# Kernel tuning notes

Measured on AMD Instinct MI355X. Metric: run time of the kernel, lower is better.

## Reference

```python
import jax, jax.numpy as jnp
import numpy as np

B, C, H, W = 4, 256, 96, 96
PARA, MOD, NH = 256, 256, 128
PI = 3.14159  # constant used in the torch source (not math.pi)


def setup_inputs():
    key = jax.random.key(0)
    ks = jax.random.split(key, 16)
    w = lambda k, shp: jax.random.normal(k, shp, jnp.float32) * 0.02
    z = lambda n: jnp.zeros((n,), jnp.float32)
    return {
        "feature_map": jax.random.normal(ks[0], (B, C, H, W), jnp.float32),
        "para_code": jax.random.normal(ks[1], (B, PARA), jnp.float32),
        "style_code": jax.random.normal(ks[2], (B, MOD), jnp.float32),
        "lin_common_w": w(ks[3], (PARA, PARA)), "lin_common_b": z(PARA),
        "lin_scale_w": w(ks[4], (PARA, C)), "lin_scale_b": z(C),
        "lin_rot_w": w(ks[5], (PARA, C)), "lin_rot_b": z(C),
        "lin_trans_w": w(ks[6], (PARA, 2 * C)), "lin_trans_b": z(2 * C),
        "a1_shared_w": w(ks[7], (MOD, NH)), "a1_shared_b": z(NH),
        "a1_gamma_w": w(ks[8], (NH, C)), "a1_gamma_b": z(C),
        "a1_beta_w": w(ks[9], (NH, C)), "a1_beta_b": z(C),
        "conv1_w": w(ks[10], (C, C, 3, 3)), "conv1_b": z(C),
        "a2_shared_w": w(ks[11], (MOD, NH)), "a2_shared_b": z(NH),
        "a2_gamma_w": w(ks[12], (NH, C)), "a2_gamma_b": z(C),
        "a2_beta_w": w(ks[13], (NH, C)), "a2_beta_b": z(C),
        "conv2_w": w(ks[14], (C, C, 3, 3)), "conv2_b": z(C),
    }


def _adaat(fm, pc, cw, cb, sw, sb, rw, rb, tw, tb):
    # fm: [B,C,H,W]; per-channel 2D affine warp, channels act as depth of a 3D grid_sample.
    Bn, Cn, Hn, Wn = fm.shape
    pc = jax.nn.relu(pc @ cw + cb)
    scale = jax.nn.sigmoid(pc @ sw + sb) * 2.0            # [B,C]
    angle = jnp.tanh(pc @ rw + rb) * PI                   # [B,C]
    trans = jnp.tanh(pc @ tw + tb).reshape(Bn, Cn, 2)     # [B,C,2]
    cos = jnp.cos(angle)[:, :, None, None]
    sin = jnp.sin(angle)[:, :, None, None]
    sc = scale[:, :, None, None]
    tx = trans[:, :, 0][:, :, None, None]
    ty = trans[:, :, 1][:, :, None, None]
    # align_corners=True style normalized source grid (as in make_coordinate_grid_3d)
    gx = (2.0 * jnp.arange(Wn) / (Wn - 1) - 1.0)[None, :]  # [1,W]
    gy = (2.0 * jnp.arange(Hn) / (Hn - 1) - 1.0)[:, None]  # [H,1]
    # rotation [[cos,-sin],[sin,cos]] @ [x,y], then scale + translate -> [B,C,H,W]
    xw = (cos * gx - sin * gy) * sc + tx
    yw = (sin * gx + cos * gy) * sc + ty
    gz = 2.0 * jnp.arange(Cn) / (Cn - 1) - 1.0             # [C]
    # unnormalize with align_corners=False (torch grid_sample default)
    ix = ((xw + 1.0) * Wn - 1.0) * 0.5
    iy = ((yw + 1.0) * Hn - 1.0) * 0.5
    iz = (((gz + 1.0) * Cn - 1.0) * 0.5)[None, :, None, None]  # [1,C,1,1]
    x0 = jnp.floor(ix); y0 = jnp.floor(iy); z0 = jnp.floor(iz)
    wx = ix - x0; wy = iy - y0; wz = iz - z0
    x0 = x0.astype(jnp.int32); y0 = y0.astype(jnp.int32); z0 = z0.astype(jnp.int32)
    bidx = jnp.arange(Bn)[:, None, None, None]

    def gather(zi, yi, xi):
        valid = (zi >= 0) & (zi < Cn) & (yi >= 0) & (yi < Hn) & (xi >= 0) & (xi < Wn)
        v = fm[bidx, jnp.clip(zi, 0, Cn - 1), jnp.clip(yi, 0, Hn - 1), jnp.clip(xi, 0, Wn - 1)]
        return jnp.where(valid, v, 0.0)

    out = jnp.zeros_like(fm)
    for dz, wzc in ((0, 1.0 - wz), (1, wz)):
        for dy, wyc in ((0, 1.0 - wy), (1, wy)):
            for dx, wxc in ((0, 1.0 - wx), (1, wx)):
                out = out + gather(z0 + dz, y0 + dy, x0 + dx) * (wzc * wyc * wxc)
    return out


def _adain_layer(x, style, shw, shb, gw, gb, bw, bb):
    m = x.mean(axis=(2, 3), keepdims=True)
    v = x.var(axis=(2, 3), keepdims=True)  # biased, as torch InstanceNorm2d
    xn = (x - m) / jnp.sqrt(v + 1e-5)
    a = jax.nn.relu(style @ shw + shb)
    gamma = (a @ gw + gb)[:, :, None, None]
    beta = (a @ bw + bb)[:, :, None, None]
    return xn * (1.0 + gamma) + beta


def _conv3(x, w, b):
    y = jax.lax.conv_general_dilated(x, w, (1, 1), ((1, 1), (1, 1)),
                                     dimension_numbers=("NCHW", "OIHW", "NCHW"))
    return y + b[None, :, None, None]


def _lrelu(x):
    return jnp.where(x >= 0, x, 0.2 * x)


def reference(feature_map, para_code, style_code,
              lin_common_w, lin_common_b, lin_scale_w, lin_scale_b,
              lin_rot_w, lin_rot_b, lin_trans_w, lin_trans_b,
              a1_shared_w, a1_shared_b, a1_gamma_w, a1_gamma_b, a1_beta_w, a1_beta_b,
              conv1_w, conv1_b,
              a2_shared_w, a2_shared_b, a2_gamma_w, a2_gamma_b, a2_beta_w, a2_beta_b,
              conv2_w, conv2_b):
    t = _adaat(feature_map, para_code, lin_common_w, lin_common_b,
               lin_scale_w, lin_scale_b, lin_rot_w, lin_rot_b, lin_trans_w, lin_trans_b)
    x = _adain_layer(t, style_code, a1_shared_w, a1_shared_b, a1_gamma_w, a1_gamma_b, a1_beta_w, a1_beta_b)
    x = _conv3(_lrelu(x), conv1_w, conv1_b)
    x = _adain_layer(x, style_code, a2_shared_w, a2_shared_b, a2_gamma_w, a2_gamma_b, a2_beta_w, a2_beta_b)
    x = _conv3(_lrelu(x), conv2_w, conv2_b)
    return x
```

## Files before the change

### kernel.cpp

```cpp
#include <hip/hip_runtime.h>
#include <hip/hip_bf16.h>
#include <cstddef>

#define BATCH 4
#define CH 256
#define HH 96
#define WW 96
#define HWN (HH*WW)
#define NTOT (BATCH*CH*HWN)
#define XT_H 98
#define XT_W 98
#define XT_PLANE (XT_H*XT_W*CH)

typedef __attribute__((ext_vector_type(16))) float f32x16;
typedef __attribute__((ext_vector_type(8))) __bf16 bfrag;
typedef __attribute__((ext_vector_type(8))) unsigned short u16x8;

static __device__ __forceinline__ unsigned short f2bf(float f) {
  unsigned int u = __float_as_uint(f);
  unsigned int r = (u + 0x7fffu + ((u >> 16) & 1u)) >> 16;
  return (unsigned short)r;
}
static __device__ __forceinline__ float bf2f(unsigned short s) {
  return __uint_as_float(((unsigned int)s) << 16);
}

static __device__ __forceinline__ void gload16(const unsigned short* g,
                                               unsigned short* l) {
  __builtin_amdgcn_global_load_lds(
      (const __attribute__((address_space(1))) unsigned int*)g,
      (__attribute__((address_space(3))) unsigned int*)l, 16, 0, 0);
}

__global__ __launch_bounds__(256) void params_stage1_kernel(
    const float* __restrict__ para, const float* __restrict__ style,
    const float* __restrict__ cw,  const float* __restrict__ cb,
    const float* __restrict__ a1w, const float* __restrict__ a1b,
    const float* __restrict__ a2w, const float* __restrict__ a2b,
    float* __restrict__ pcbuf, float* __restrict__ a1buf, float* __restrict__ a2buf)
{
  __shared__ float s_in[256];
  __shared__ float red[256];
  int part = blockIdx.x, b = blockIdx.y, t = threadIdx.x;
  s_in[t] = (part < 4) ? para[b*256 + t] : style[b*256 + t];
  __syncthreads();
  if (part < 4) {
    int o = t & 63, ks = t >> 6, co0 = part * 64;
    const float* wcol = cw + co0 + o;
    float acc = 0.f;
    #pragma unroll 8
    for (int i = 0; i < 64; i++) {
      int k = ks * 64 + i;
      acc = fmaf(s_in[k], wcol[k * 256], acc);
    }
    red[t] = acc;
    __syncthreads();
    if (t < 64) {
      float s = red[t] + red[t + 64] + red[t + 128] + red[t + 192];
      pcbuf[b*256 + co0 + t] = fmaxf(s + cb[co0 + t], 0.f);
    }
  } else {
    const float* w  = (part == 4) ? a1w : a2w;
    const float* bb = (part == 4) ? a1b : a2b;
    float* outp = (part == 4) ? a1buf : a2buf;
    int o = t & 127, ks = t >> 7;
    const float* wcol = w + o;
    float acc = 0.f;
    #pragma unroll 8
    for (int i = 0; i < 128; i++) {
      int k = ks * 128 + i;
      acc = fmaf(s_in[k], wcol[k * 128], acc);
    }
    red[t] = acc;
    __syncthreads();
    if (t < 128) {
      float s = red[t] + red[t + 128];
      outp[b*128 + t] = fmaxf(s + bb[t], 0.f);
    }
  }
}

__global__ __launch_bounds__(256) void params_stage2_kernel(
    const float* __restrict__ pcbuf, const float* __restrict__ a1buf,
    const float* __restrict__ a2buf,
    const float* __restrict__ sw,  const float* __restrict__ sb,
    const float* __restrict__ rw,  const float* __restrict__ rb,
    const float* __restrict__ tw,  const float* __restrict__ tb,
    const float* __restrict__ g1w, const float* __restrict__ g1b,
    const float* __restrict__ b1w, const float* __restrict__ b1b,
    const float* __restrict__ g2w, const float* __restrict__ g2b,
    const float* __restrict__ b2w, const float* __restrict__ b2b,
    float* __restrict__ warp, float* __restrict__ gb1, float* __restrict__ gb2)
{
  __shared__ float s_pc[256], s_a1[128], s_a2[128];
  __shared__ float red[8][4][16];
  int co0 = blockIdx.x * 16, b = blockIdx.y, t = threadIdx.x;
  s_pc[t] = pcbuf[b*256 + t];
  if (t < 128) s_a1[t] = a1buf[b*128 + t];
  else         s_a2[t - 128] = a2buf[b*128 + (t - 128)];
  __syncthreads();

  int cl = t & 15, klane = t >> 4;
  int c = co0 + cl;
  const float2* tw2 = (const float2*)tw;
  float ds = 0.f, dr = 0.f, dtx = 0.f, dty = 0.f;
  float g1 = 0.f, be1 = 0.f, g2 = 0.f, be2 = 0.f;
  #pragma unroll 4
  for (int kk = 0; kk < 16; kk++) {
    int i = klane * 16 + kk;
    float p = s_pc[i];
    ds  = fmaf(p, sw[i*256 + c], ds);
    dr  = fmaf(p, rw[i*256 + c], dr);
    float2 tv = tw2[i*256 + c];
    dtx = fmaf(p, tv.x, dtx);
    dty = fmaf(p, tv.y, dty);
  }
  #pragma unroll 4
  for (int kk = 0; kk < 8; kk++) {
    int i = klane * 8 + kk;
    float a = s_a1[i];
    g1  = fmaf(a, g1w[i*256 + c], g1);
    be1 = fmaf(a, b1w[i*256 + c], be1);
    float a2v = s_a2[i];
    g2  = fmaf(a2v, g2w[i*256 + c], g2);
    be2 = fmaf(a2v, b2w[i*256 + c], be2);
  }
  ds  += __shfl_down(ds, 32, 64);  ds  += __shfl_down(ds, 16, 64);
  dr  += __shfl_down(dr, 32, 64);  dr  += __shfl_down(dr, 16, 64);
  dtx += __shfl_down(dtx, 32, 64); dtx += __shfl_down(dtx, 16, 64);
  dty += __shfl_down(dty, 32, 64); dty += __shfl_down(dty, 16, 64);
  g1  += __shfl_down(g1, 32, 64);  g1  += __shfl_down(g1, 16, 64);
  be1 += __shfl_down(be1, 32, 64); be1 += __shfl_down(be1, 16, 64);
  g2  += __shfl_down(g2, 32, 64);  g2  += __shfl_down(g2, 16, 64);
  be2 += __shfl_down(be2, 32, 64); be2 += __shfl_down(be2, 16, 64);
  int wv = t >> 6;
  if ((t & 63) < 16) {
    red[0][wv][cl] = ds;  red[1][wv][cl] = dr;
    red[2][wv][cl] = dtx; red[3][wv][cl] = dty;
    red[4][wv][cl] = g1;  red[5][wv][cl] = be1;
    red[6][wv][cl] = g2;  red[7][wv][cl] = be2;
  }
  __syncthreads();
  if (t < 16) {
    float v[8];
    #pragma unroll
    for (int o = 0; o < 8; o++)
      v[o] = red[o][0][t] + red[o][1][t] + red[o][2][t] + red[o][3][t];
    int cc = co0 + t;
    int bc = b*256 + cc;
    float scale = 2.f / (1.f + expf(-(v[0] + sb[cc])));
    float ang = tanhf(v[1] + rb[cc]) * 3.14159f;
    float sn, cs;
    sincosf(ang, &sn, &cs);
    warp[bc*4 + 0] = cs * scale;
    warp[bc*4 + 1] = sn * scale;
    warp[bc*4 + 2] = tanhf(v[2] + tb[2*cc]);
    warp[bc*4 + 3] = tanhf(v[3] + tb[2*cc + 1]);
    gb1[bc*2]     = v[4] + g1b[cc];
    gb1[bc*2 + 1] = v[5] + b1b[cc];
    gb2[bc*2]     = v[6] + g2b[cc];
    gb2[bc*2 + 1] = v[7] + b2b[cc];
  }
}

__global__ __launch_bounds__(256) void prep_weights_kernel(
    const float* __restrict__ w1, const float* __restrict__ w2,
    unsigned short* __restrict__ wf1, unsigned short* __restrict__ wf2)
{
  int co = blockIdx.x & 255;
  const float* src = (blockIdx.x < 256) ? w1 : w2;
  unsigned short* dst = (blockIdx.x < 256) ? wf1 : wf2;
  int ci = threadIdx.x;
  int coblk = co >> 6, m = (co >> 5) & 1;
  int l = (co & 31) | (((ci >> 3) & 1) << 5);
  int ks = ci >> 4, j = ci & 7;
  const float* p = src + ((size_t)co * 256 + ci) * 9;
  #pragma unroll
  for (int tap = 0; tap < 9; tap++) {
    size_t idx = (((size_t)((coblk * 16 + ks) * 9 + tap) * 2 + m) * 64 + l) * 8 + j;
    dst[idx] = f2bf(p[tap]);
  }
}

__global__ __launch_bounds__(256) void adaat_kernel(
    const float* __restrict__ fm, const float* __restrict__ warp,
    const float* __restrict__ gb1, float* __restrict__ tout,
    float* __restrict__ nrm1)
{
  __shared__ float s[96 * 100];
  int bc = blockIdx.x;
  int b = bc >> 8, c = bc & 255;
  float csc = warp[bc*4 + 0], ssc = warp[bc*4 + 1];
  float tx = warp[bc*4 + 2], ty = warp[bc*4 + 3];

  const float axw = csc * (96.f / 95.f);
  const float axh = -ssc * (96.f / 95.f);
  const float ax0 = 48.f * (tx - csc + ssc) + 47.5f;
  const float ayw = ssc * (96.f / 95.f);
  const float ayh = csc * (96.f / 95.f);
  const float ay0 = 48.f * (ty - ssc - csc) + 47.5f;

  float iz = 256.f * (float)c / 255.f - 0.5f;
  float z0f = floorf(iz);
  float wz = iz - z0f;
  int z0 = (int)z0f;
  const float* p0 = (z0 >= 0) ? fm + (size_t)(b*256 + z0) * HWN : nullptr;
  const float* p1 = (z0 + 1 < 256) ? fm + (size_t)(b*256 + z0 + 1) * HWN : nullptr;
  float w0 = 1.f - wz, w1 = wz;

  int t = threadIdx.x;
  const float4* q0 = (const float4*)p0;
  const float4* q1 = (const float4*)p1;
  for (int i = t; i < 2304; i += 256) {
    int row = i / 24, col = i - row * 24;
    float4 r = {0.f, 0.f, 0.f, 0.f};
    if (q0) {
      float4 v = q0[i];
      r.x = w0 * v.x; r.y = w0 * v.y; r.z = w0 * v.z; r.w = w0 * v.w;
    }
    if (q1) {
      float4 v = q1[i];
      r.x = fmaf(w1, v.x, r.x); r.y = fmaf(w1, v.y, r.y);
      r.z = fmaf(w1, v.z, r.z); r.w = fmaf(w1, v.w, r.w);
    }
    *(float4*)&s[row * 100 + col * 4] = r;
  }
  __syncthreads();

  int h = t / 96, w = t - (t / 96) * 96;
  float* dst = tout + (size_t)bc * HWN;
  float sum = 0.f, sumsq = 0.f;
  #pragma unroll
  for (int k = 0; k < 36; k++) {
    float ix = fmaf(axw, (float)w, fmaf(axh, (float)h, ax0));
    float iy = fmaf(ayw, (float)w, fmaf(ayh, (float)h, ay0));
    float x0f = floorf(ix), y0f = floorf(iy);
    float wx = ix - x0f, wy = iy - y0f;
    int x0 = (int)x0f, y0 = (int)y0f;
    int x0c = min(max(x0, 0), 95), x1c = min(max(x0 + 1, 0), 95);
    int y0c = min(max(y0, 0), 95), y1c = min(max(y0 + 1, 0), 95);
    bool vx0 = (unsigned)x0 < 96u, vx1 = (unsigned)(x0 + 1) < 96u;
    bool vy0 = (unsigned)y0 < 96u, vy1 = (unsigned)(y0 + 1) < 96u;
    float a00 = s[y0c * 100 + x0c], a01 = s[y0c * 100 + x1c];
    float a10 = s[y1c * 100 + x0c], a11 = s[y1c * 100 + x1c];
    float wxm = 1.f - wx, wym = 1.f - wy;
    float w00 = (vy0 && vx0) ? wym * wxm : 0.f;
    float w01 = (vy0 && vx1) ? wym * wx  : 0.f;
    float w10 = (vy1 && vx0) ? wy * wxm  : 0.f;
    float w11 = (vy1 && vx1) ? wy * wx   : 0.f;
    float v = w00 * a00;
    v = fmaf(w01, a01, v);
    v = fmaf(w10, a10, v);
    v = fmaf(w11, a11, v);
    dst[t + k * 256] = v;
    sum += v;
    sumsq = fmaf(v, v, sumsq);
    int wn = w + 64;
    int carry = (wn >= 96) ? 1 : 0;
    w = wn - (carry ? 96 : 0);
    h += 2 + carry;
  }

  for (int off = 32; off > 0; off >>= 1) {
    sum   += __shfl_down(sum, off, 64);
    sumsq += __shfl_down(sumsq, off, 64);
  }
  __shared__ float rs[4], rq[4];
  int lane = t & 63, wvi = t >> 6;
  if (lane == 0) { rs[wvi] = sum; rq[wvi] = sumsq; }
  __syncthreads();
  if (t == 0) {
    float S = rs[0] + rs[1] + rs[2] + rs[3];
    float Q = rq[0] + rq[1] + rq[2] + rq[3];
    float m = S * (1.f / 9216.f);
    float var = Q * (1.f / 9216.f) - m * m;
    float rstd = rsqrtf(var + 1e-5f);
    float sc = (1.f + gb1[bc*2]) * rstd;
    nrm1[bc*2] = sc;
    nrm1[bc*2 + 1] = gb1[bc*2 + 1] - m * sc;
  }
}

__global__ __launch_bounds__(256) void finalize_stats_kernel(
    const float* __restrict__ psum, const float* __restrict__ gb,
    float* __restrict__ nrm)
{
  int bc = blockIdx.x * 256 + threadIdx.x;
  int b = bc >> 8, co = bc & 255;
  float S = 0.f, Q = 0.f;
  for (int j = 0; j < 96; j++) {
    const float* p = psum + ((((size_t)b * 48 + (j >> 1)) * 2 + (j & 1)) * 256 + co) * 2;
    S += p[0];
    Q += p[1];
  }
  float m = S * (1.f / 9216.f);
  float var = Q * (1.f / 9216.f) - m * m;
  float rstd = rsqrtf(var + 1e-5f);
  float sc = (1.f + gb[bc*2]) * rstd;
  nrm[bc*2] = sc;
  nrm[bc*2 + 1] = gb[bc*2 + 1] - m * sc;
}

__global__ __launch_bounds__(256) void transpose_norm_kernel(
    const float* __restrict__ x, const float* __restrict__ nrm,
    unsigned short* __restrict__ xt)
{
  int hi = blockIdx.x;
  int b  = blockIdx.y;
  unsigned short* dst = xt + (size_t)b * XT_PLANE + (size_t)hi * (XT_W * CH);
  int t = threadIdx.x;
  int h = hi - 1;
  u16x8 zero = {0,0,0,0,0,0,0,0};
  if (h < 0 || h >= 96) {
    for (int c = t; c < XT_W * CH / 8; c += 256) ((u16x8*)dst)[c] = zero;
    return;
  }
  __shared__ unsigned short s[96 * 256];
  int ci = t;
  float sc = nrm[(b*256 + ci)*2], bi = nrm[(b*256 + ci)*2 + 1];
  const float* src = x + ((size_t)(b*256 + ci)) * HWN + h * 96;
  for (int wg = 0; wg < 24; wg++) {
    float4 v = *(const float4*)(src + wg * 4);
    float y0 = fmaf(v.x, sc, bi); y0 = (y0 >= 0.f) ? y0 : 0.2f * y0;
    float y1 = fmaf(v.y, sc, bi); y1 = (y1 >= 0.f) ? y1 : 0.2f * y1;
    float y2 = fmaf(v.z, sc, bi); y2 = (y2 >= 0.f) ? y2 : 0.2f * y2;
    float y3 = fmaf(v.w, sc, bi); y3 = (y3 >= 0.f) ? y3 : 0.2f * y3;
    s[(wg*4 + 0) * 256 + ci] = f2bf(y0);
    s[(wg*4 + 1) * 256 + ci] = f2bf(y1);
    s[(wg*4 + 2) * 256 + ci] = f2bf(y2);
    s[(wg*4 + 3) * 256 + ci] = f2bf(y3);
  }
  __syncthreads();
  for (int c = t; c < 98 * 32; c += 256) {
    int w = c >> 5, p = c & 31;
    u16x8 v = zero;
    if (w >= 1 && w <= 96) v = *(const u16x8*)&s[(w - 1) * 256 + p * 8];
    ((u16x8*)dst)[c] = v;
  }
}

__global__ __launch_bounds__(256) void norm2_kernel(
    unsigned short* __restrict__ xt, const float* __restrict__ nrm)
{
  int hi = blockIdx.x, b = blockIdx.y;
  unsigned short* row = xt + (size_t)b * XT_PLANE + (size_t)hi * (XT_W * CH);
  int t = threadIdx.x;
  u16x8 zero = {0,0,0,0,0,0,0,0};
  if (hi == 0 || hi == 97) {
    for (int c = t; c < XT_W * CH / 8; c += 256) ((u16x8*)row)[c] = zero;
    return;
  }
  int p = t & 31;
  float sc[8], bi[8];
  #pragma unroll
  for (int j = 0; j < 8; j++) {
    int co = p * 8 + j;
    sc[j] = nrm[(b*256 + co)*2];
    bi[j] = nrm[(b*256 + co)*2 + 1];
  }
  for (int wi = t >> 5; wi < 98; wi += 8) {
    int c = wi * 32 + p;
    if (wi == 0 || wi == 97) { ((u16x8*)row)[c] = zero; continue; }
    u16x8 v = ((u16x8*)row)[c];
    u16x8 o;
    #pragma unroll
    for (int j = 0; j < 8; j++) {
      float x = bf2f(v[j]);
      float y = fmaf(x, sc[j], bi[j]);
      y = (y >= 0.f) ? y : 0.2f * y;
      o[j] = f2bf(y);
    }
    ((u16x8*)row)[c] = o;
  }
}

__global__ __launch_bounds__(256, 3) void conv_mfma_kernel(
    const unsigned short* __restrict__ xt,
    const unsigned short* __restrict__ wf,
    const float* __restrict__ cb,
    float* __restrict__ out,
    unsigned short* __restrict__ xt2,
    float* __restrict__ psum)
{
  __shared__ __align__(16) unsigned short s_in[2][6528];

  int hb = blockIdx.x, coblk = blockIdx.y, b = blockIdx.z;
  int co0 = coblk * 64, h0 = hb * 2;
  int t = threadIdx.x, lane = t & 63, wv = t >> 6;
  int rw = wv >> 1, mh = wv & 1;
  int l31 = lane & 31, lhi = lane >> 5;
  const unsigned short* xtb = xt + (size_t)b * XT_PLANE;

  int pre_g[4];
  #pragma unroll
  for (int i = 0; i < 4; i++) {
    int c = t + i * 256;
    if (c < 784) {
      int r = c / 196;
      int rem = c - r * 196;
      int half = rem / 98;
      int w = rem - half * 98;
      pre_g[i] = ((h0 + r) * 98 + w) * 256 + half * 8;
    }
  }

  f32x16 acc[3];
  #pragma unroll
  for (int n = 0; n < 3; n++)
    #pragma unroll
    for (int i = 0; i < 16; i++) acc[n][i] = 0.f;

  const unsigned short* wfb = wf + (size_t)(coblk * 16) * 9216 + mh * 512 + lane * 8;

  {
    #pragma unroll
    for (int i = 0; i < 3; i++)
      gload16(xtb + pre_g[i], &s_in[0][(i * 256 + wv * 64) * 8]);
    u16x8 tail0;
    if (t < 16) tail0 = *(const u16x8*)(xtb + pre_g[3]);
    if (t < 16) *(u16x8*)(&s_in[0][(768 + t) * 8]) = tail0;
  }
  bfrag wa[9];
  #pragma unroll
  for (int tap = 0; tap < 9; tap++) wa[tap] = *(const bfrag*)(wfb + tap * 1024);
  __syncthreads();

  int buf = 0;
  u16x8 tail;
  #pragma unroll 1
  for (int ks = 0; ks < 16; ks++) {
    if (ks < 15) {
      int cib = (ks + 1) * 16;
      unsigned short* nb = s_in[buf ^ 1];
      #pragma unroll
      for (int i = 0; i < 3; i++)
        gload16(xtb + pre_g[i] + cib, &nb[(i * 256 + wv * 64) * 8]);
      if (t < 16) tail = *(const u16x8*)(xtb + pre_g[3] + cib);
    }
    const unsigned short* sb = s_in[buf];
    int ksn = (ks < 15) ? (ks + 1) : 15;
    const unsigned short* wkn = wfb + (size_t)ksn * 9216;
    #pragma unroll
    for (int ky = 0; ky < 3; ky++) {
      const unsigned short* srow = sb + (((rw + ky) * 2 + lhi) * 98) * 8;
      bfrag bb[9];
      #pragma unroll
      for (int kx = 0; kx < 3; kx++)
        #pragma unroll
        for (int n = 0; n < 3; n++)
          bb[kx * 3 + n] = *(const bfrag*)(srow + (n * 32 + kx + l31) * 8);
      __builtin_amdgcn_s_setprio(1);
      #pragma unroll
      for (int kx = 0; kx < 3; kx++) {
        int tap = ky * 3 + kx;
        acc[0] = __builtin_amdgcn_mfma_f32_32x32x16_bf16(wa[tap], bb[kx*3+0], acc[0], 0, 0, 0);
        acc[1] = __builtin_amdgcn_mfma_f32_32x32x16_bf16(wa[tap], bb[kx*3+1], acc[1], 0, 0, 0);
        acc[2] = __builtin_amdgcn_mfma_f32_32x32x16_bf16(wa[tap], bb[kx*3+2], acc[2], 0, 0, 0);
        wa[tap] = *(const bfrag*)(wkn + tap * 1024);
      }
      __builtin_amdgcn_s_setprio(0);
    }
    if (ks < 15 && t < 16) *(u16x8*)(&s_in[buf ^ 1][(768 + t) * 8]) = tail;
    __syncthreads();
    buf ^= 1;
  }

  int h = h0 + rw;
  if (psum) {
    unsigned short* tb = (unsigned short*)s_in;
    float bsum[16], bsq[16];
    #pragma unroll
    for (int r = 0; r < 16; r++) {
      int row = (r & 3) + 8 * (r >> 2) + 4 * lhi;
      int col = mh * 32 + row;
      float bv = cb[co0 + col];
      float s = 0.f, q = 0.f;
      #pragma unroll
      for (int n = 0; n < 3; n++) {
        float y = acc[n][r] + bv;
        int px = n * 32 + l31;
        tb[(rw * 96 + px) * 68 + col] = f2bf(y);
        s += y;
        q = fmaf(y, y, q);
      }
      bsum[r] = s; bsq[r] = q;
    }
    #pragma unroll
    for (int r = 0; r < 16; r++) {
      float s = bsum[r], q = bsq[r];
      #pragma unroll
      for (int off = 16; off > 0; off >>= 1) {
        s += __shfl_xor(s, off, 64);
        q += __shfl_xor(q, off, 64);
      }
      bsum[r] = s; bsq[r] = q;
    }
    if (l31 == 0) {
      float* pp = psum + ((((size_t)b * 48 + hb) * 2 + rw) * 256) * 2;
      #pragma unroll
      for (int r = 0; r < 16; r++) {
        int row = (r & 3) + 8 * (r >> 2) + 4 * lhi;
        int co = co0 + mh * 32 + row;
        pp[co * 2]     = bsum[r];
        pp[co * 2 + 1] = bsq[r];
      }
    }
    __syncthreads();
    unsigned short* dstb = xt2 + (size_t)b * XT_PLANE;
    #pragma unroll
    for (int i = 0; i < 6; i++) {
      int c = t + i * 256;
      int row2 = c / 768;
      int rem = c - row2 * 768;
      int wi = rem >> 3, p8 = rem & 7;
      const unsigned short* lsrc = &tb[(row2 * 96 + wi) * 68 + p8 * 8];
      uint2 lo = *(const uint2*)lsrc;
      uint2 hi2 = *(const uint2*)(lsrc + 4);
      size_t ga = ((size_t)(h0 + 1 + row2) * 98 + (wi + 1)) * 256 + co0 + p8 * 8;
      uint4 vv; vv.x = lo.x; vv.y = lo.y; vv.z = hi2.x; vv.w = hi2.y;
      *(uint4*)&dstb[ga] = vv;
    }
  } else {
    #pragma unroll
    for (int r = 0; r < 16; r++) {
      int row = (r & 3) + 8 * (r >> 2) + 4 * lhi;
      int co = co0 + mh * 32 + row;
      float bv = cb[co];
      size_t base = ((size_t)(b * 256 + co) * 96 + h) * 96;
      #pragma unroll
      for (int n = 0; n < 3; n++) {
        out[base + n * 32 + l31] = acc[n][r] + bv;
      }
    }
  }
}

extern "C" void kernel_launch(void* const* d_in, const int* in_sizes, int n_in,
                              void* d_out, int out_size, void* d_ws, size_t ws_size,
                              hipStream_t stream)
{
  const float* fm    = (const float*)d_in[0];
  const float* para  = (const float*)d_in[1];
  const float* style = (const float*)d_in[2];
  const float* cw  = (const float*)d_in[3];
  const float* cb  = (const float*)d_in[4];
  const float* sw  = (const float*)d_in[5];
  const float* sb  = (const float*)d_in[6];
  const float* rw  = (const float*)d_in[7];
  const float* rb  = (const float*)d_in[8];
  const float* tw  = (const float*)d_in[9];
  const float* tb  = (const float*)d_in[10];
  const float* a1w = (const float*)d_in[11];
  const float* a1b = (const float*)d_in[12];
  const float* g1w = (const float*)d_in[13];
  const float* g1b = (const float*)d_in[14];
  const float* b1w = (const float*)d_in[15];
  const float* b1b = (const float*)d_in[16];
  const float* c1w = (const float*)d_in[17];
  const float* c1b = (const float*)d_in[18];
  const float* a2w = (const float*)d_in[19];
  const float* a2b = (const float*)d_in[20];
  const float* g2w = (const float*)d_in[21];
  const float* g2b = (const float*)d_in[22];
  const float* b2w = (const float*)d_in[23];
  const float* b2b = (const float*)d_in[24];
  const float* c2w = (const float*)d_in[25];
  const float* c2b = (const float*)d_in[26];

  float* outf = (float*)d_out;

  unsigned short* xtbuf  = (unsigned short*)d_ws;
  unsigned short* xt2buf = xtbuf + (size_t)BATCH * XT_PLANE;
  unsigned short* wf1    = xt2buf + (size_t)BATCH * XT_PLANE;
  unsigned short* wf2    = wf1 + 9 * 256 * 256;
  float* fws  = (float*)(wf2 + 9 * 256 * 256);
  float* warp = fws;
  float* gb1  = warp + 4 * 1024;
  float* gb2  = gb1 + 2 * 1024;
  float* nrm1 = gb2 + 2 * 1024;
  float* nrm2 = nrm1 + 2 * 1024;
  float* pcbuf = nrm2 + 2 * 1024;
  float* a1buf = pcbuf + 1024;
  float* a2buf = a1buf + 512;
  float* psum  = a2buf + 512;

  params_stage1_kernel<<<dim3(6, 4), 256, 0, stream>>>(para, style, cw, cb,
      a1w, a1b, a2w, a2b, pcbuf, a1buf, a2buf);
  params_stage2_kernel<<<dim3(16, 4), 256, 0, stream>>>(pcbuf, a1buf, a2buf,
      sw, sb, rw, rb, tw, tb, g1w, g1b, b1w, b1b, g2w, g2b, b2w, b2b,
      warp, gb1, gb2);
  prep_weights_kernel<<<512, 256, 0, stream>>>(c1w, c2w, wf1, wf2);
  adaat_kernel<<<1024, 256, 0, stream>>>(fm, warp, gb1, outf, nrm1);
  transpose_norm_kernel<<<dim3(98, 4), 256, 0, stream>>>(outf, nrm1, xtbuf);
  conv_mfma_kernel<<<dim3(48, 4, 4), 256, 0, stream>>>(xtbuf, wf1, c1b,
      outf, xt2buf, psum);
  finalize_stats_kernel<<<4, 256, 0, stream>>>(psum, gb2, nrm2);
  norm2_kernel<<<dim3(98, 4), 256, 0, stream>>>(xt2buf, nrm2);
  conv_mfma_kernel<<<dim3(48, 4, 4), 256, 0, stream>>>(xt2buf, wf2, c2b,
      outf, nullptr, nullptr);
}
```

Baseline: 185.1 us.

## Fuse AdaIN-1 normalize into adaat kernel, store bf16, remap conv block order

The adaat kernel now keeps its 36 warped values per thread in registers. After the block reduction it applies the AdaIN scale/bias and leaky ReLU itself, then writes bf16 instead of fp32. The transpose kernel becomes a pure bf16 transpose, which halves the intermediate traffic, and the nrm1 buffer is removed. The conv kernels switch to a 1D grid with a custom index decode that interleaves co-blocks and batch pairs, aiming at better L2 reuse of input rows and weights. The cost is higher register pressure in the adaat kernel and bf16 rounding earlier in the pipeline.

```diff
diff --git a/kernel.cpp b/kernel.cpp
--- a/kernel.cpp
+++ b/kernel.cpp
@@ -184,8 +184,7 @@
 
 __global__ __launch_bounds__(256) void adaat_kernel(
     const float* __restrict__ fm, const float* __restrict__ warp,
-    const float* __restrict__ gb1, float* __restrict__ tout,
-    float* __restrict__ nrm1)
+    const float* __restrict__ gb1, unsigned short* __restrict__ tout)
 {
   __shared__ float s[96 * 100];
   int bc = blockIdx.x;
@@ -228,7 +227,7 @@
   __syncthreads();
 
   int h = t / 96, w = t - (t / 96) * 96;
-  float* dst = tout + (size_t)bc * HWN;
+  float vals[36];
   float sum = 0.f, sumsq = 0.f;
   #pragma unroll
   for (int k = 0; k < 36; k++) {
@@ -252,7 +251,7 @@
     v = fmaf(w01, a01, v);
     v = fmaf(w10, a10, v);
     v = fmaf(w11, a11, v);
-    dst[t + k * 256] = v;
+    vals[k] = v;
     sum += v;
     sumsq = fmaf(v, v, sumsq);
     int wn = w + 64;
@@ -265,7 +264,7 @@
     sum   += __shfl_down(sum, off, 64);
     sumsq += __shfl_down(sumsq, off, 64);
   }
-  __shared__ float rs[4], rq[4];
+  __shared__ float rs[4], rq[4], sbi[2];
   int lane = t & 63, wvi = t >> 6;
   if (lane == 0) { rs[wvi] = sum; rq[wvi] = sumsq; }
   __syncthreads();
@@ -276,8 +275,17 @@
     float var = Q * (1.f / 9216.f) - m * m;
     float rstd = rsqrtf(var + 1e-5f);
     float sc = (1.f + gb1[bc*2]) * rstd;
-    nrm1[bc*2] = sc;
-    nrm1[bc*2 + 1] = gb1[bc*2 + 1] - m * sc;
+    sbi[0] = sc;
+    sbi[1] = gb1[bc*2 + 1] - m * sc;
+  }
+  __syncthreads();
+  float sc = sbi[0], bi = sbi[1];
+  unsigned short* dst = tout + (size_t)bc * HWN + t;
+  #pragma unroll
+  for (int k = 0; k < 36; k++) {
+    float y = fmaf(vals[k], sc, bi);
+    y = (y >= 0.f) ? y : 0.2f * y;
+    dst[k * 256] = f2bf(y);
   }
 }
 
@@ -301,9 +309,8 @@
   nrm[bc*2 + 1] = gb[bc*2 + 1] - m * sc;
 }
 
-__global__ __launch_bounds__(256) void transpose_norm_kernel(
-    const float* __restrict__ x, const float* __restrict__ nrm,
-    unsigned short* __restrict__ xt)
+__global__ __launch_bounds__(256) void transpose_kernel(
+    const unsigned short* __restrict__ tb, unsigned short* __restrict__ xt)
 {
   int hi = blockIdx.x;
   int b  = blockIdx.y;
@@ -317,18 +324,12 @@
   }
   __shared__ unsigned short s[96 * 256];
   int ci = t;
-  float sc = nrm[(b*256 + ci)*2], bi = nrm[(b*256 + ci)*2 + 1];
-  const float* src = x + ((size_t)(b*256 + ci)) * HWN + h * 96;
-  for (int wg = 0; wg < 24; wg++) {
-    float4 v = *(const float4*)(src + wg * 4);
-    float y0 = fmaf(v.x, sc, bi); y0 = (y0 >= 0.f) ? y0 : 0.2f * y0;
-    float y1 = fmaf(v.y, sc, bi); y1 = (y1 >= 0.f) ? y1 : 0.2f * y1;
-    float y2 = fmaf(v.z, sc, bi); y2 = (y2 >= 0.f) ? y2 : 0.2f * y2;
-    float y3 = fmaf(v.w, sc, bi); y3 = (y3 >= 0.f) ? y3 : 0.2f * y3;
-    s[(wg*4 + 0) * 256 + ci] = f2bf(y0);
-    s[(wg*4 + 1) * 256 + ci] = f2bf(y1);
-    s[(wg*4 + 2) * 256 + ci] = f2bf(y2);
-    s[(wg*4 + 3) * 256 + ci] = f2bf(y3);
+  const unsigned short* src = tb + ((size_t)(b*256 + ci)) * HWN + h * 96;
+  #pragma unroll
+  for (int wg = 0; wg < 12; wg++) {
+    u16x8 v = *(const u16x8*)(src + wg * 8);
+    #pragma unroll
+    for (int j = 0; j < 8; j++) s[(wg*8 + j) * 256 + ci] = v[j];
   }
   __syncthreads();
   for (int c = t; c < 98 * 32; c += 256) {
@@ -384,7 +385,13 @@
 {
   __shared__ __align__(16) unsigned short s_in[2][6528];
 
-  int hb = blockIdx.x, coblk = blockIdx.y, b = blockIdx.z;
+  int n = blockIdx.x;
+  int coblk = n & 3;
+  int bit2 = (n >> 2) & 1;
+  int j = n >> 3;
+  int hb = j % 48;
+  int b = (j / 48) * 2 + bit2;
+
   int co0 = coblk * 64, h0 = hb * 2;
   int t = threadIdx.x, lane = t & 63, wv = t >> 6;
   int rw = wv >> 1, mh = wv & 1;
@@ -406,9 +413,9 @@
 
   f32x16 acc[3];
   #pragma unroll
-  for (int n = 0; n < 3; n++)
-    #pragma unroll
-    for (int i = 0; i < 16; i++) acc[n][i] = 0.f;
+  for (int nn = 0; nn < 3; nn++)
+    #pragma unroll
+    for (int i = 0; i < 16; i++) acc[nn][i] = 0.f;
 
   const unsigned short* wfb = wf + (size_t)(coblk * 16) * 9216 + mh * 512 + lane * 8;
 
@@ -447,8 +454,8 @@
       #pragma unroll
       for (int kx = 0; kx < 3; kx++)
         #pragma unroll
-        for (int n = 0; n < 3; n++)
-          bb[kx * 3 + n] = *(const bfrag*)(srow + (n * 32 + kx + l31) * 8);
+        for (int nn = 0; nn < 3; nn++)
+          bb[kx * 3 + nn] = *(const bfrag*)(srow + (nn * 32 + kx + l31) * 8);
       __builtin_amdgcn_s_setprio(1);
       #pragma unroll
       for (int kx = 0; kx < 3; kx++) {
@@ -467,7 +474,7 @@
 
   int h = h0 + rw;
   if (psum) {
-    unsigned short* tb = (unsigned short*)s_in;
+    unsigned short* tbl = (unsigned short*)s_in;
     float bsum[16], bsq[16];
     #pragma unroll
     for (int r = 0; r < 16; r++) {
@@ -476,10 +483,10 @@
       float bv = cb[co0 + col];
       float s = 0.f, q = 0.f;
       #pragma unroll
-      for (int n = 0; n < 3; n++) {
-        float y = acc[n][r] + bv;
-        int px = n * 32 + l31;
-        tb[(rw * 96 + px) * 68 + col] = f2bf(y);
+      for (int nn = 0; nn < 3; nn++) {
+        float y = acc[nn][r] + bv;
+        int px = nn * 32 + l31;
+        tbl[(rw * 96 + px) * 68 + col] = f2bf(y);
         s += y;
         q = fmaf(y, y, q);
       }
@@ -513,7 +520,7 @@
       int row2 = c / 768;
       int rem = c - row2 * 768;
       int wi = rem >> 3, p8 = rem & 7;
-      const unsigned short* lsrc = &tb[(row2 * 96 + wi) * 68 + p8 * 8];
+      const unsigned short* lsrc = &tbl[(row2 * 96 + wi) * 68 + p8 * 8];
       uint2 lo = *(const uint2*)lsrc;
       uint2 hi2 = *(const uint2*)(lsrc + 4);
       size_t ga = ((size_t)(h0 + 1 + row2) * 98 + (wi + 1)) * 256 + co0 + p8 * 8;
@@ -528,8 +535,8 @@
       float bv = cb[co];
       size_t base = ((size_t)(b * 256 + co) * 96 + h) * 96;
       #pragma unroll
-      for (int n = 0; n < 3; n++) {
-        out[base + n * 32 + l31] = acc[n][r] + bv;
+      for (int nn = 0; nn < 3; nn++) {
+        out[base + nn * 32 + l31] = acc[nn][r] + bv;
       }
     }
   }
@@ -568,6 +575,7 @@
   const float* c2b = (const float*)d_in[26];
 
   float* outf = (float*)d_out;
+  unsigned short* tbf16 = (unsigned short*)d_out;
 
   unsigned short* xtbuf  = (unsigned short*)d_ws;
   unsigned short* xt2buf = xtbuf + (size_t)BATCH * XT_PLANE;
@@ -577,8 +585,7 @@
   float* warp = fws;
   float* gb1  = warp + 4 * 1024;
   float* gb2  = gb1 + 2 * 1024;
-  float* nrm1 = gb2 + 2 * 1024;
-  float* nrm2 = nrm1 + 2 * 1024;
+  float* nrm2 = gb2 + 2 * 1024;
   float* pcbuf = nrm2 + 2 * 1024;
   float* a1buf = pcbuf + 1024;
   float* a2buf = a1buf + 512;
@@ -590,12 +597,12 @@
       sw, sb, rw, rb, tw, tb, g1w, g1b, b1w, b1b, g2w, g2b, b2w, b2b,
       warp, gb1, gb2);
   prep_weights_kernel<<<512, 256, 0, stream>>>(c1w, c2w, wf1, wf2);
-  adaat_kernel<<<1024, 256, 0, stream>>>(fm, warp, gb1, outf, nrm1);
-  transpose_norm_kernel<<<dim3(98, 4), 256, 0, stream>>>(outf, nrm1, xtbuf);
-  conv_mfma_kernel<<<dim3(48, 4, 4), 256, 0, stream>>>(xtbuf, wf1, c1b,
+  adaat_kernel<<<1024, 256, 0, stream>>>(fm, warp, gb1, tbf16);
+  transpose_kernel<<<dim3(98, 4), 256, 0, stream>>>(tbf16, xtbuf);
+  conv_mfma_kernel<<<768, 256, 0, stream>>>(xtbuf, wf1, c1b,
       outf, xt2buf, psum);
   finalize_stats_kernel<<<4, 256, 0, stream>>>(psum, gb2, nrm2);
   norm2_kernel<<<dim3(98, 4), 256, 0, stream>>>(xt2buf, nrm2);
-  conv_mfma_kernel<<<dim3(48, 4, 4), 256, 0, stream>>>(xt2buf, wf2, c2b,
+  conv_mfma_kernel<<<768, 256, 0, stream>>>(xt2buf, wf2, c2b,
       outf, nullptr, nullptr);
 }
```

Measured after the change: 183.5 us. About the same (-0.8%).
